# Kernel tuning notes

Hardware: AMD Instinct MI355X
Metric: run time of the kernel (lower is better)

The kernel has to match this reference:

```python
import jax, jax.numpy as jnp
import numpy as np

IGNORE_INDEX = -100
SMOOTHING = 0.2


def setup_inputs() -> dict:
    key = jax.random.key(0)
    k1, k2, k3 = jax.random.split(key, 3)
    B, C = 524288, 170  # ~0.5M frames, 170 chord classes
    logits = jax.random.normal(k1, (B, C), dtype=jnp.float32)
    targets = jax.random.randint(k2, (B,), 0, C)
    # similarity values in [0,1); rows sum > 0 so normalization is safe
    sim_matrix = jax.random.uniform(k3, (C, C), dtype=jnp.float32)
    return {"logits": logits, "targets": targets, "sim_matrix": sim_matrix}


def reference(logits, targets, sim_matrix):
    B, C = logits.shape
    valid = targets != IGNORE_INDEX                      # [B]
    t = jnp.where(valid, targets, 0)                     # safe gather index

    # vectorized gather + row-normalize (replaces per-sample python loop)
    rows = sim_matrix[t]                                 # [B, C]
    rows = rows / rows.sum(axis=1, keepdims=True)

    one_hot = jax.nn.one_hot(t, C, dtype=logits.dtype)   # [B, C]
    soft = (1.0 - SMOOTHING) * one_hot + SMOOTHING * rows
    soft = soft * valid[:, None].astype(logits.dtype)    # ignored rows -> all zeros

    log_probs = jax.nn.log_softmax(logits, axis=1)

    # F.kl_div(log_probs, soft, reduction='batchmean'):
    # sum(soft * (log(soft) - log_probs)) / B, with 0*log(0) := 0
    pos = soft > 0
    safe_soft = jnp.where(pos, soft, 1.0)
    kl = jnp.where(pos, soft * (jnp.log(safe_soft) - log_probs), 0.0)
    loss = kl.sum() / B
    return jnp.maximum(loss, 0.0)
```

## Files before the change

### kernel.cpp

```cpp
#include <hip/hip_runtime.h>
#include <cmath>

#define IGNORE_INDEX (-100)
#define SMOOTHING 0.2f

__device__ __forceinline__ float wave_reduce_max(float v) {
#pragma unroll
    for (int off = 32; off > 0; off >>= 1)
        v = fmaxf(v, __shfl_xor(v, off, 64));
    return v;
}
__device__ __forceinline__ float wave_reduce_sum(float v) {
#pragma unroll
    for (int off = 32; off > 0; off >>= 1)
        v += __shfl_xor(v, off, 64);
    return v;
}

__global__ void prep_kernel(const float* __restrict__ sim, float* __restrict__ S,
                            float* __restrict__ H, float* __restrict__ acc, int C) {
    const int c = blockIdx.x;
    const int lane = threadIdx.x;
    if (c == 0 && lane == 0) acc[0] = 0.f;

    float psum = 0.f;
    for (int j = lane; j < C; j += 64) psum += sim[(size_t)c * C + j];
    const float inv = 1.f / wave_reduce_sum(psum);

    float h = 0.f;
    for (int j = lane; j < C; j += 64) {
        float s = SMOOTHING * sim[(size_t)c * C + j] * inv + ((j == c) ? (1.f - SMOOTHING) : 0.f);
        S[(size_t)c * C + j] = s;
        if (s > 0.f) h += s * logf(s);
    }
    h = wave_reduce_sum(h);
    if (lane == 0) H[c] = h;
}

__global__ __launch_bounds__(256) void main_kernel(
    const float* __restrict__ logits, const int* __restrict__ targets,
    const float* __restrict__ S, const float* __restrict__ H,
    float* __restrict__ acc, int Bn, int C) {
    const int lane = threadIdx.x & 63;
    const int wid = threadIdx.x >> 6;
    const int wave = blockIdx.x * 4 + wid;
    const int nwaves = gridDim.x * 4;
    const int n2 = C >> 1;
    const bool has2 = (lane + 64) < n2;

    float wsum = 0.f;
    for (int i = wave; i < Bn; i += nwaves) {
        const int t = targets[i];
        if (t == IGNORE_INDEX) continue;

        const float2* xr = (const float2*)(logits + (size_t)i * C);
        const float2* sr = (const float2*)(S + (size_t)t * C);
        float2 xa = xr[lane];
        float2 sa = sr[lane];
        float2 xb = make_float2(-INFINITY, -INFINITY);
        float2 sb = make_float2(0.f, 0.f);
        if (has2) { xb = xr[lane + 64]; sb = sr[lane + 64]; }

        float m = fmaxf(fmaxf(xa.x, xa.y), fmaxf(xb.x, xb.y));
        m = wave_reduce_max(m);

        float se = __expf(xa.x - m) + __expf(xa.y - m);
        float dot = sa.x * xa.x + sa.y * xa.y;
        if (has2) {
            se += __expf(xb.x - m) + __expf(xb.y - m);
            dot += sb.x * xb.x + sb.y * xb.y;
        }
        se = wave_reduce_sum(se);
        dot = wave_reduce_sum(dot);

        const float lse = m + __logf(se);
        wsum += H[t] - dot + lse;
    }

    __shared__ float wsums[4];
    if (lane == 0) wsums[wid] = wsum;
    __syncthreads();
    if (threadIdx.x == 0)
        atomicAdd(acc, wsums[0] + wsums[1] + wsums[2] + wsums[3]);
}

__global__ void finish_kernel(const float* __restrict__ acc, float* __restrict__ out,
                              float invB) {
    if (threadIdx.x == 0 && blockIdx.x == 0)
        out[0] = fmaxf(acc[0] * invB, 0.f);
}

extern "C" void kernel_launch(void* const* d_in, const int* in_sizes, int n_in,
                              void* d_out, int out_size, void* d_ws, size_t ws_size,
                              hipStream_t stream) {
    const float* logits = (const float*)d_in[0];
    const int* targets = (const int*)d_in[1];
    const float* sim = (const float*)d_in[2];
    float* out = (float*)d_out;

    const int Bn = in_sizes[1];
    const int C = in_sizes[0] / Bn;

    char* ws = (char*)d_ws;
    float* S = (float*)ws;
    float* H = (float*)(ws + (size_t)C * C * sizeof(float));
    size_t off = ((size_t)C * C + (size_t)C) * sizeof(float);
    off = (off + 255) & ~(size_t)255;
    float* acc = (float*)(ws + off);

    prep_kernel<<<C, 64, 0, stream>>>(sim, S, H, acc, C);

    main_kernel<<<2048, 256, 0, stream>>>(logits, targets, S, H, acc, Bn, C);

    finish_kernel<<<1, 64, 0, stream>>>(acc, out, 1.0f / (float)Bn);
}
```

Before: 529.3 us.

## Process two rows per wave with contiguous chunks and deferred dot reduction

Each wave now handles a contiguous chunk of rows instead of a grid-stride loop, and processes two rows per iteration so their loads and shuffle reductions can interleave. The per-row dot-product reduction is replaced by a per-lane accumulator that is reduced once at the end, removing one wave reduction per row. Ignored rows are masked rather than skipped, which adds some wasted loads but makes control flow uniform across the wave.

```diff
diff --git a/kernel.cpp b/kernel.cpp
--- a/kernel.cpp
+++ b/kernel.cpp
@@ -45,37 +45,99 @@
     const int wid = threadIdx.x >> 6;
     const int wave = blockIdx.x * 4 + wid;
     const int nwaves = gridDim.x * 4;
+    const int spw = (Bn + nwaves - 1) / nwaves;
+    const int start = wave * spw;
+    const int end = (start + spw < Bn) ? (start + spw) : Bn;
+
     const int n2 = C >> 1;
     const bool has2 = (lane + 64) < n2;
 
-    float wsum = 0.f;
-    for (int i = wave; i < Bn; i += nwaves) {
-        const int t = targets[i];
-        if (t == IGNORE_INDEX) continue;
+    float dotacc = 0.f;
+    float usum = 0.f;
 
-        const float2* xr = (const float2*)(logits + (size_t)i * C);
-        const float2* sr = (const float2*)(S + (size_t)t * C);
-        float2 xa = xr[lane];
-        float2 sa = sr[lane];
-        float2 xb = make_float2(-INFINITY, -INFINITY);
-        float2 sb = make_float2(0.f, 0.f);
-        if (has2) { xb = xr[lane + 64]; sb = sr[lane + 64]; }
+    int i = start;
+    for (; i + 1 < end; i += 2) {
+        const int t0 = targets[i];
+        const int t1 = targets[i + 1];
+        const bool v0 = (t0 != IGNORE_INDEX);
+        const bool v1 = (t1 != IGNORE_INDEX);
+        const int i0 = v0 ? t0 : 0;
+        const int i1 = v1 ? t1 : 0;
 
-        float m = fmaxf(fmaxf(xa.x, xa.y), fmaxf(xb.x, xb.y));
-        m = wave_reduce_max(m);
+        const float2* xr0 = (const float2*)(logits + (size_t)i * C);
+        const float2* xr1 = (const float2*)(logits + (size_t)(i + 1) * C);
+        const float2* sr0 = (const float2*)(S + (size_t)i0 * C);
+        const float2* sr1 = (const float2*)(S + (size_t)i1 * C);
 
-        float se = __expf(xa.x - m) + __expf(xa.y - m);
-        float dot = sa.x * xa.x + sa.y * xa.y;
+        float2 x0a = xr0[lane];
+        float2 x1a = xr1[lane];
+        float2 s0a = sr0[lane];
+        float2 s1a = sr1[lane];
+        float2 x0b = make_float2(-INFINITY, -INFINITY);
+        float2 x1b = make_float2(-INFINITY, -INFINITY);
+        float2 s0b = make_float2(0.f, 0.f);
+        float2 s1b = make_float2(0.f, 0.f);
         if (has2) {
-            se += __expf(xb.x - m) + __expf(xb.y - m);
-            dot += sb.x * xb.x + sb.y * xb.y;
+            x0b = xr0[lane + 64]; s0b = sr0[lane + 64];
+            x1b = xr1[lane + 64]; s1b = sr1[lane + 64];
         }
-        se = wave_reduce_sum(se);
-        dot = wave_reduce_sum(dot);
 
-        const float lse = m + __logf(se);
-        wsum += H[t] - dot + lse;
+        float m0 = fmaxf(fmaxf(x0a.x, x0a.y), fmaxf(x0b.x, x0b.y));
+        float m1 = fmaxf(fmaxf(x1a.x, x1a.y), fmaxf(x1b.x, x1b.y));
+#pragma unroll
+        for (int off = 32; off > 0; off >>= 1) {
+            m0 = fmaxf(m0, __shfl_xor(m0, off, 64));
+            m1 = fmaxf(m1, __shfl_xor(m1, off, 64));
+        }
+
+        float se0 = __expf(x0a.x - m0) + __expf(x0a.y - m0);
+        float se1 = __expf(x1a.x - m1) + __expf(x1a.y - m1);
+        if (has2) {
+            se0 += __expf(x0b.x - m0) + __expf(x0b.y - m0);
+            se1 += __expf(x1b.x - m1) + __expf(x1b.y - m1);
+        }
+#pragma unroll
+        for (int off = 32; off > 0; off >>= 1) {
+            se0 += __shfl_xor(se0, off, 64);
+            se1 += __shfl_xor(se1, off, 64);
+        }
+
+        float d0 = s0a.x * x0a.x + s0a.y * x0a.y;
+        float d1 = s1a.x * x1a.x + s1a.y * x1a.y;
+        if (has2) {
+            d0 += s0b.x * x0b.x + s0b.y * x0b.y;
+            d1 += s1b.x * x1b.x + s1b.y * x1b.y;
+        }
+        dotacc += (v0 ? d0 : 0.f) + (v1 ? d1 : 0.f);
+
+        usum += (v0 ? (H[i0] + m0 + __logf(se0)) : 0.f)
+              + (v1 ? (H[i1] + m1 + __logf(se1)) : 0.f);
     }
+    for (; i < end; ++i) {
+        const int t0 = targets[i];
+        const bool v0 = (t0 != IGNORE_INDEX);
+        const int i0 = v0 ? t0 : 0;
+        const float2* xr0 = (const float2*)(logits + (size_t)i * C);
+        const float2* sr0 = (const float2*)(S + (size_t)i0 * C);
+        float2 x0a = xr0[lane];
+        float2 s0a = sr0[lane];
+        float2 x0b = make_float2(-INFINITY, -INFINITY);
+        float2 s0b = make_float2(0.f, 0.f);
+        if (has2) { x0b = xr0[lane + 64]; s0b = sr0[lane + 64]; }
+        float m0 = fmaxf(fmaxf(x0a.x, x0a.y), fmaxf(x0b.x, x0b.y));
+        m0 = wave_reduce_max(m0);
+        float se0 = __expf(x0a.x - m0) + __expf(x0a.y - m0);
+        float d0 = s0a.x * x0a.x + s0a.y * x0a.y;
+        if (has2) {
+            se0 += __expf(x0b.x - m0) + __expf(x0b.y - m0);
+            d0 += s0b.x * x0b.x + s0b.y * x0b.y;
+        }
+        se0 = wave_reduce_sum(se0);
+        dotacc += v0 ? d0 : 0.f;
+        usum += v0 ? (H[i0] + m0 + __logf(se0)) : 0.f;
+    }
+
+    const float wsum = usum - wave_reduce_sum(dotacc);
 
     __shared__ float wsums[4];
     if (lane == 0) wsums[wid] = wsum;
```

Result: no change. 525.8 us (-0.7%).

## Process four rows per wave with 16-lane groups and contiguous row chunks

Applied to the files above, without the earlier changes.

Adds a kernel templated on class count that splits each 64-lane wave into four 16-lane groups, each handling one row. The compile-time class count lets the per-lane loads be fully unrolled. Each wave now walks a contiguous chunk of rows instead of striding across the batch, and the per-row dot products are accumulated and reduced only once at the end. This is meant to cut idle lanes (the old mapping left many lanes unused for 85 float2 elements) and the number of full-wave shuffle reductions per row. In exchange, each lane holds more registers, and the short 16-lane reductions plus the bounds masking add instructions. A generic fallback kernel covers other class counts.

```diff
diff --git a/kernel.cpp b/kernel.cpp
--- a/kernel.cpp
+++ b/kernel.cpp
@@ -37,7 +37,80 @@
     if (lane == 0) H[c] = h;
 }
 
-__global__ __launch_bounds__(256) void main_kernel(
+template <int CC>
+__global__ __launch_bounds__(256) void main_kernel_t(
+    const float* __restrict__ logits, const int* __restrict__ targets,
+    const float* __restrict__ S, const float* __restrict__ H,
+    float* __restrict__ acc, int Bn) {
+    constexpr int NF2 = CC / 2;
+    constexpr int NCH = (NF2 + 15) / 16;
+
+    const int lane = threadIdx.x & 63;
+    const int wid  = threadIdx.x >> 6;
+    const int wave = blockIdx.x * 4 + wid;
+    const int nwaves = gridDim.x * 4;
+    const int spw = (Bn + nwaves - 1) / nwaves;
+    const int start = wave * spw;
+    const int end = (start + spw < Bn) ? (start + spw) : Bn;
+
+    const int g = lane >> 4;
+    const int u = lane & 15;
+
+    float dotacc = 0.f;
+    float usum   = 0.f;
+
+    for (int i = start; i < end; i += 4) {
+        const int s_idx = i + g;
+        const bool in_range = (s_idx < end);
+        const int t = in_range ? targets[s_idx] : IGNORE_INDEX;
+        const bool v = in_range && (t != IGNORE_INDEX);
+        const int cls = v ? t : 0;
+
+        const float2* xr = (const float2*)(logits + (size_t)(in_range ? s_idx : start) * CC);
+        const float2* sr = (const float2*)(S + (size_t)cls * CC);
+
+        float2 x[NCH], sv[NCH];
+#pragma unroll
+        for (int c = 0; c < NCH; ++c) {
+            const bool ok = (c * 16 + u < NF2) && in_range;
+            x[c]  = ok ? xr[c * 16 + u] : make_float2(-INFINITY, -INFINITY);
+            sv[c] = ok ? sr[c * 16 + u] : make_float2(0.f, 0.f);
+        }
+
+        float m = -INFINITY;
+#pragma unroll
+        for (int c = 0; c < NCH; ++c) m = fmaxf(m, fmaxf(x[c].x, x[c].y));
+#pragma unroll
+        for (int off = 8; off >= 1; off >>= 1)
+            m = fmaxf(m, __shfl_xor(m, off, 64));
+
+        float se = 0.f, d = 0.f;
+#pragma unroll
+        for (int c = 0; c < NCH; ++c) {
+            se += __expf(x[c].x - m) + __expf(x[c].y - m);
+            const bool ok = (c * 16 + u < NF2) && in_range;
+            d += ok ? (sv[c].x * x[c].x + sv[c].y * x[c].y) : 0.f;
+        }
+#pragma unroll
+        for (int off = 8; off >= 1; off >>= 1)
+            se += __shfl_xor(se, off, 64);
+
+        dotacc += v ? d : 0.f;
+        const float lse = m + __logf(se);
+        usum += (v && u == 0) ? (H[cls] + lse) : 0.f;
+    }
+
+    float tot = usum - dotacc;
+    tot = wave_reduce_sum(tot);
+
+    __shared__ float wsums[4];
+    if (lane == 0) wsums[wid] = tot;
+    __syncthreads();
+    if (threadIdx.x == 0)
+        atomicAdd(acc, wsums[0] + wsums[1] + wsums[2] + wsums[3]);
+}
+
+__global__ __launch_bounds__(256) void main_kernel_gen(
     const float* __restrict__ logits, const int* __restrict__ targets,
     const float* __restrict__ S, const float* __restrict__ H,
     float* __restrict__ acc, int Bn, int C) {
@@ -45,38 +118,26 @@
     const int wid = threadIdx.x >> 6;
     const int wave = blockIdx.x * 4 + wid;
     const int nwaves = gridDim.x * 4;
-    const int n2 = C >> 1;
-    const bool has2 = (lane + 64) < n2;
 
     float wsum = 0.f;
     for (int i = wave; i < Bn; i += nwaves) {
         const int t = targets[i];
-        if (t == IGNORE_INDEX) continue;
-
-        const float2* xr = (const float2*)(logits + (size_t)i * C);
-        const float2* sr = (const float2*)(S + (size_t)t * C);
-        float2 xa = xr[lane];
-        float2 sa = sr[lane];
-        float2 xb = make_float2(-INFINITY, -INFINITY);
-        float2 sb = make_float2(0.f, 0.f);
-        if (has2) { xb = xr[lane + 64]; sb = sr[lane + 64]; }
-
-        float m = fmaxf(fmaxf(xa.x, xa.y), fmaxf(xb.x, xb.y));
+        const bool v = (t != IGNORE_INDEX);
+        const int cls = v ? t : 0;
+        const float* xr = logits + (size_t)i * C;
+        const float* sr = S + (size_t)cls * C;
+        float m = -INFINITY;
+        for (int j = lane; j < C; j += 64) m = fmaxf(m, xr[j]);
         m = wave_reduce_max(m);
-
-        float se = __expf(xa.x - m) + __expf(xa.y - m);
-        float dot = sa.x * xa.x + sa.y * xa.y;
-        if (has2) {
-            se += __expf(xb.x - m) + __expf(xb.y - m);
-            dot += sb.x * xb.x + sb.y * xb.y;
+        float se = 0.f, d = 0.f;
+        for (int j = lane; j < C; j += 64) {
+            se += __expf(xr[j] - m);
+            d += sr[j] * xr[j];
         }
         se = wave_reduce_sum(se);
-        dot = wave_reduce_sum(dot);
-
-        const float lse = m + __logf(se);
-        wsum += H[t] - dot + lse;
+        d = wave_reduce_sum(d);
+        wsum += v ? (H[cls] + m + __logf(se) - d) : 0.f;
     }
-
     __shared__ float wsums[4];
     if (lane == 0) wsums[wid] = wsum;
     __syncthreads();
@@ -110,7 +171,11 @@
 
     prep_kernel<<<C, 64, 0, stream>>>(sim, S, H, acc, C);
 
-    main_kernel<<<2048, 256, 0, stream>>>(logits, targets, S, H, acc, Bn, C);
+    if (C == 170) {
+        main_kernel_t<170><<<2048, 256, 0, stream>>>(logits, targets, S, H, acc, Bn);
+    } else {
+        main_kernel_gen<<<2048, 256, 0, stream>>>(logits, targets, S, H, acc, Bn, C);
+    }
 
     finish_kernel<<<1, 64, 0, stream>>>(acc, out, 1.0f / (float)Bn);
 }
```

New measurement: 494.5 us. 6.6% less time.
